# Kernel tuning notes

Measured on AMD Instinct MI355X. Metric: run time of the kernel, lower is better.

The kernel has to match this reference:

```python
import jax, jax.numpy as jnp
import numpy as np

VOCAB, E, HID, T = 100000, 256, 512, 12
H = HID // 2          # per-direction LSTM hidden
B, S = 64, 256
START, STOP = 10, 11  # tag_to_ix['<START>'], tag_to_ix['<STOP>']
NEG = -10000.0


def setup_inputs() -> dict:
    key = jax.random.key(0)
    ks = jax.random.split(key, 16)
    inp = {
        'batch_sentence': jax.random.randint(ks[0], (B, S), 0, VOCAB),
        'sentence_length': S,
        'batch_chars2': jnp.zeros((1,), jnp.int64 if jax.config.jax_enable_x64 else jnp.int32),
        'chars2_length': 1,
        'emb': jax.random.normal(ks[1], (VOCAB, E), jnp.float32),
        # PyTorch LSTM layout: W_ih [4H, in], W_hh [4H, H], gate order i,f,g,o
        'Wih_f': jax.random.normal(ks[2], (4 * H, E), jnp.float32) * 0.05,
        'Whh_f': jax.random.normal(ks[3], (4 * H, H), jnp.float32) * 0.05,
        'bih_f': jnp.zeros((4 * H,), jnp.float32),
        'bhh_f': jnp.zeros((4 * H,), jnp.float32),
        'Wih_b': jax.random.normal(ks[4], (4 * H, E), jnp.float32) * 0.05,
        'Whh_b': jax.random.normal(ks[5], (4 * H, H), jnp.float32) * 0.05,
        'bih_b': jnp.zeros((4 * H,), jnp.float32),
        'bhh_b': jnp.zeros((4 * H,), jnp.float32),
        'Wt': jax.random.normal(ks[6], (T, HID), jnp.float32) * 0.05,
        'bt': jnp.zeros((T,), jnp.float32),
        'transitions': jax.random.normal(ks[7], (T, T), jnp.float32),
        # init_hidden() draws randn hidden state: h0/c0 [2 dirs, B, H]
        'h0': jax.random.normal(ks[8], (2, B, H), jnp.float32),
        'c0': jax.random.normal(ks[9], (2, B, H), jnp.float32),
    }
    return inp


def _lstm(x, h0, c0, Wih, Whh, bih, bhh):
    # x: [S, B, E] -> hs: [S, B, H]
    def step(carry, xt):
        h, c = carry
        g = xt @ Wih.T + h @ Whh.T + (bih + bhh)
        i, f, gg, o = jnp.split(g, 4, axis=-1)
        c = jax.nn.sigmoid(f) * c + jax.nn.sigmoid(i) * jnp.tanh(gg)
        h = jax.nn.sigmoid(o) * jnp.tanh(c)
        return (h, c), h
    _, hs = jax.lax.scan(step, (h0, c0), x)
    return hs


def _viterbi(feats, transitions):
    # feats: [S, T] emissions for one sequence
    init = jnp.full((T,), NEG, feats.dtype).at[START].set(0.0)

    def step(fv, feat):
        scores = fv[None, :] + transitions            # [next_tag, prev_tag]
        new_fv = jnp.max(scores, axis=1) + feat       # best prev per next
        bptr = jnp.argmax(scores, axis=1)
        return new_fv, bptr

    fv, bptrs = jax.lax.scan(step, init, feats)       # bptrs: [S, T]
    term = fv + transitions[STOP]
    term = term.at[STOP].set(NEG).at[START].set(NEG)  # torch code masks these
    last = jnp.argmax(term)
    score = term[last]

    def back(tag, bptr):
        return bptr[tag], tag                          # y_t = tag at time t
    _, path = jax.lax.scan(back, last, bptrs, reverse=True)
    return score, path


def reference(batch_sentence, sentence_length, batch_chars2, chars2_length,
              emb, Wih_f, Whh_f, bih_f, bhh_f, Wih_b, Whh_b, bih_b, bhh_b,
              Wt, bt, transitions, h0, c0):
    # word embeddings (dropout = identity at inference)
    x = emb[batch_sentence].transpose(1, 0, 2)        # [S, B, E]
    hf = _lstm(x, h0[0], c0[0], Wih_f, Whh_f, bih_f, bhh_f)
    hb = _lstm(x[::-1], h0[1], c0[1], Wih_b, Whh_b, bih_b, bhh_b)[::-1]
    out = jnp.concatenate([hf, hb], axis=-1)          # [S, B, HID]
    feats = out @ Wt.T + bt                           # [S, B, T]
    feats = feats.transpose(1, 0, 2)                  # [B, S, T]
    scores, paths = jax.vmap(_viterbi, in_axes=(0, None))(feats, transitions)
    return scores, paths
```

## Files before the change

kernel.cpp:

```cpp
#include <hip/hip_runtime.h>
#include <cstdint>
#include <cstddef>

#define EDIM 256
#define HID  512
#define NTAG 12
#define HDIM 256
#define BB   64
#define SS   256
#define START_TAG 10
#define STOP_TAG  11
#define NEGV (-10000.0f)
#define UPW  8

typedef __attribute__((ext_vector_type(8))) short bf16x8;
typedef __attribute__((ext_vector_type(4))) float f32x4;

__device__ __forceinline__ unsigned short bf16_rne(float x) {
  union { float f; unsigned u; } a; a.f = x;
  return (unsigned short)((a.u + 0x7fffu + ((a.u >> 16) & 1u)) >> 16);
}
__device__ __forceinline__ float bf16_tof(unsigned short h) {
  union { unsigned u; float f; } a; a.u = ((unsigned)h) << 16; return a.f;
}
__device__ __forceinline__ void unpack8(const unsigned* u, bf16x8& hi, bf16x8& lo) {
#pragma unroll
  for (int j = 0; j < 8; ++j) {
    hi[j] = (short)(u[j] & 0xffffu);
    lo[j] = (short)(u[j] >> 16);
  }
}
__device__ __forceinline__ void pack_hilo(const float* xf, bf16x8& hi, bf16x8& lo) {
#pragma unroll
  for (int j = 0; j < 8; ++j) {
    unsigned short hb = bf16_rne(xf[j]);
    hi[j] = (short)hb;
    lo[j] = (short)bf16_rne(xf[j] - bf16_tof(hb));
  }
}

__global__ void k0_gather(const int* __restrict__ sent,
                          const float* __restrict__ emb,
                          unsigned int* __restrict__ xpk) {
  int t = blockIdx.x;
  for (int n = threadIdx.x; n < BB * EDIM; n += 256) {
    int b = n >> 8, k = n & 255;
    int tok = sent[b * SS + t];
    float x = emb[(size_t)tok * EDIM + k];
    unsigned short hb = bf16_rne(x);
    unsigned short lb = bf16_rne(x - bf16_tof(hb));
    xpk[((size_t)t * BB + b) * EDIM + k] = (unsigned)hb | ((unsigned)lb << 16);
  }
}

__global__ void __launch_bounds__(256, 1)
lstm_fused(const float* __restrict__ WhhF, const float* __restrict__ WhhB,
           const float* __restrict__ WihF, const float* __restrict__ WihB,
           const float* __restrict__ bihF, const float* __restrict__ bhhF,
           const float* __restrict__ bihB, const float* __restrict__ bhhB,
           const unsigned int* __restrict__ xpk,
           const float* __restrict__ h0, const float* __restrict__ c0,
           float* __restrict__ hseq, unsigned int* __restrict__ hx) {
  const int bid = blockIdx.x;
  const int d = bid >> 5, w = bid & 31;
  const int tid = threadIdx.x;
  const int lane = tid & 63;
  const int v = tid >> 6;
  const int l15 = lane & 15, l4 = lane >> 4;
  const int bcol = v * 16 + l15;
  const int u2 = ((l4 & 1) << 2) | ((l4 >> 1) << 1);
  const bool low = (l4 < 2);
  const int kg0 = w * UPW + u2;
  const float* Whh = d ? WhhB : WhhF;
  const float* Wih = d ? WihB : WihF;
  const float* bi  = d ? bihB : bihF;
  const float* bh  = d ? bhhB : bhhF;

  bf16x8 Hhi[2][8], Hlo[2][8], Xhi[2][8], Xlo[2][8];
#pragma unroll
  for (int rt = 0; rt < 2; ++rt) {
    int i = rt * 16 + l15;
    int R = ((i >> 3) << 8) + w * UPW + (i & 7);
    const float* wrow = Whh + (size_t)R * HDIM;
    const float* xrow = Wih + (size_t)R * EDIM;
#pragma unroll
    for (int kk = 0; kk < 8; ++kk) {
      {
        float4 f0 = *(const float4*)(wrow + kk * 32 + l4 * 8);
        float4 f1 = *(const float4*)(wrow + kk * 32 + l4 * 8 + 4);
        float xf[8] = {f0.x, f0.y, f0.z, f0.w, f1.x, f1.y, f1.z, f1.w};
        pack_hilo(xf, Hhi[rt][kk], Hlo[rt][kk]);
      }
      {
        float4 f0 = *(const float4*)(xrow + kk * 32 + l4 * 8);
        float4 f1 = *(const float4*)(xrow + kk * 32 + l4 * 8 + 4);
        float xf[8] = {f0.x, f0.y, f0.z, f0.w, f1.x, f1.y, f1.z, f1.w};
        pack_hilo(xf, Xhi[rt][kk], Xlo[rt][kk]);
      }
    }
  }
  f32x4 bias0, bias1;
#pragma unroll
  for (int r = 0; r < 4; ++r) {
    int i0 = l4 * 4 + r;
    int R0 = ((i0 >> 3) << 8) + w * UPW + (i0 & 7);
    bias0[r] = bi[R0] + bh[R0];
    int i1 = 16 + i0;
    int R1 = ((i1 >> 3) << 8) + w * UPW + (i1 & 7);
    bias1[r] = bi[R1] + bh[R1];
  }
  float c2[2];
  c2[0] = c0[((size_t)d * BB + bcol) * HDIM + kg0];
  c2[1] = c0[((size_t)d * BB + bcol) * HDIM + kg0 + 1];

  for (int s = 0; s < SS; ++s) {
    const int t = d ? (SS - 1 - s) : s;

    const unsigned int* xc = xpk + ((size_t)t * BB + bcol) * EDIM;
    uint4 xq[16];
#pragma unroll
    for (int kk = 0; kk < 8; ++kk) {
      xq[2 * kk]     = *(const uint4*)(xc + kk * 32 + l4 * 8);
      xq[2 * kk + 1] = *(const uint4*)(xc + kk * 32 + l4 * 8 + 4);
    }

    f32x4 accA = bias0, accD = bias1;
    f32x4 accB = {0.f, 0.f, 0.f, 0.f}, accC = accB, accE = accB, accF = accB;
#pragma unroll
    for (int kk = 0; kk < 8; ++kk) {
      unsigned u[8] = {xq[2 * kk].x, xq[2 * kk].y, xq[2 * kk].z, xq[2 * kk].w,
                       xq[2 * kk + 1].x, xq[2 * kk + 1].y,
                       xq[2 * kk + 1].z, xq[2 * kk + 1].w};
      bf16x8 xh, xl;
      unpack8(u, xh, xl);
      accA = __builtin_amdgcn_mfma_f32_16x16x32_bf16(Xhi[0][kk], xh, accA, 0, 0, 0);
      accB = __builtin_amdgcn_mfma_f32_16x16x32_bf16(Xhi[0][kk], xl, accB, 0, 0, 0);
      accC = __builtin_amdgcn_mfma_f32_16x16x32_bf16(Xlo[0][kk], xh, accC, 0, 0, 0);
      accD = __builtin_amdgcn_mfma_f32_16x16x32_bf16(Xhi[1][kk], xh, accD, 0, 0, 0);
      accE = __builtin_amdgcn_mfma_f32_16x16x32_bf16(Xhi[1][kk], xl, accE, 0, 0, 0);
      accF = __builtin_amdgcn_mfma_f32_16x16x32_bf16(Xlo[1][kk], xh, accF, 0, 0, 0);
    }

    unsigned uv[64];
    if (s > 0) {
      const unsigned int* slot =
          hx + ((size_t)(d * 4 + ((s - 1) & 3)) * HDIM) * BB + bcol;
      while (true) {
        int bad = 0;
#pragma unroll
        for (int kk = 0; kk < 8; ++kk)
#pragma unroll
          for (int j = 0; j < 8; ++j) {
            unsigned val = __hip_atomic_load(
                slot + (size_t)(kk * 32 + l4 * 8 + j) * BB,
                __ATOMIC_RELAXED, __HIP_MEMORY_SCOPE_AGENT);
            uv[kk * 8 + j] = val;
            bad |= (val == 0xFFFFFFFFu);
          }
        if (!__any(bad)) break;
        __builtin_amdgcn_s_sleep(1);
      }
      __builtin_amdgcn_sched_barrier(0);
    }

    {
      unsigned int* ra =
          hx + ((size_t)(d * 4 + ((s + 1) & 3)) * HDIM) * BB + bcol;
      __hip_atomic_store(ra + (size_t)kg0 * BB, 0xFFFFFFFFu,
                         __ATOMIC_RELAXED, __HIP_MEMORY_SCOPE_AGENT);
      __hip_atomic_store(ra + (size_t)(kg0 + 1) * BB, 0xFFFFFFFFu,
                         __ATOMIC_RELAXED, __HIP_MEMORY_SCOPE_AGENT);
    }

    if (s == 0) {
      const float* hrow = h0 + ((size_t)d * BB + bcol) * HDIM;
#pragma unroll
      for (int kk = 0; kk < 8; ++kk) {
        float4 f0 = *(const float4*)(hrow + kk * 32 + l4 * 8);
        float4 f1 = *(const float4*)(hrow + kk * 32 + l4 * 8 + 4);
        float xf[8] = {f0.x, f0.y, f0.z, f0.w, f1.x, f1.y, f1.z, f1.w};
        bf16x8 bhf, blf;
        pack_hilo(xf, bhf, blf);
        accA = __builtin_amdgcn_mfma_f32_16x16x32_bf16(Hhi[0][kk], bhf, accA, 0, 0, 0);
        accB = __builtin_amdgcn_mfma_f32_16x16x32_bf16(Hhi[0][kk], blf, accB, 0, 0, 0);
        accC = __builtin_amdgcn_mfma_f32_16x16x32_bf16(Hlo[0][kk], bhf, accC, 0, 0, 0);
        accD = __builtin_amdgcn_mfma_f32_16x16x32_bf16(Hhi[1][kk], bhf, accD, 0, 0, 0);
        accE = __builtin_amdgcn_mfma_f32_16x16x32_bf16(Hhi[1][kk], blf, accE, 0, 0, 0);
        accF = __builtin_amdgcn_mfma_f32_16x16x32_bf16(Hlo[1][kk], bhf, accF, 0, 0, 0);
      }
    } else {
#pragma unroll
      for (int kk = 0; kk < 8; ++kk) {
        bf16x8 bhf, blf;
        unpack8(&uv[kk * 8], bhf, blf);
        accA = __builtin_amdgcn_mfma_f32_16x16x32_bf16(Hhi[0][kk], bhf, accA, 0, 0, 0);
        accB = __builtin_amdgcn_mfma_f32_16x16x32_bf16(Hhi[0][kk], blf, accB, 0, 0, 0);
        accC = __builtin_amdgcn_mfma_f32_16x16x32_bf16(Hlo[0][kk], bhf, accC, 0, 0, 0);
        accD = __builtin_amdgcn_mfma_f32_16x16x32_bf16(Hhi[1][kk], bhf, accD, 0, 0, 0);
        accE = __builtin_amdgcn_mfma_f32_16x16x32_bf16(Hhi[1][kk], blf, accE, 0, 0, 0);
        accF = __builtin_amdgcn_mfma_f32_16x16x32_bf16(Hlo[1][kk], bhf, accF, 0, 0, 0);
      }
    }
    f32x4 acc0 = accA + accB + accC;
    f32x4 acc1 = accD + accE + accF;

    f32x4 r0, r1;
#pragma unroll
    for (int r = 0; r < 4; ++r) {
      r0[r] = __shfl_xor(acc0[r], 32);
      r1[r] = __shfl_xor(acc1[r], 32);
    }

    float hn[2]; unsigned pv[2];
#pragma unroll
    for (int e = 0; e < 2; ++e) {
      float iv = low ? acc0[e]     : r0[2 + e];
      float fv = low ? r0[e]       : acc0[2 + e];
      float gv = low ? acc1[e]     : r1[2 + e];
      float ov = low ? r1[e]       : acc1[2 + e];
      float si = 1.f / (1.f + expf(-iv));
      float sf = 1.f / (1.f + expf(-fv));
      float so = 1.f / (1.f + expf(-ov));
      float cn = sf * c2[e] + si * tanhf(gv);
      c2[e] = cn;
      float h = so * tanhf(cn);
      hn[e] = h;
      unsigned short hb2 = bf16_rne(h);
      unsigned short lb2 = bf16_rne(h - bf16_tof(hb2));
      pv[e] = (unsigned)hb2 | ((unsigned)lb2 << 16);
    }

    asm volatile("s_waitcnt vmcnt(0)" ::: "memory");

    {
      unsigned int* pd =
          hx + ((size_t)(d * 4 + (s & 3)) * HDIM) * BB + bcol;
      __hip_atomic_store(pd + (size_t)kg0 * BB, pv[0],
                         __ATOMIC_RELAXED, __HIP_MEMORY_SCOPE_AGENT);
      __hip_atomic_store(pd + (size_t)(kg0 + 1) * BB, pv[1],
                         __ATOMIC_RELAXED, __HIP_MEMORY_SCOPE_AGENT);
    }

    hseq[(((size_t)d * SS + t) * HDIM + kg0) * BB + bcol] = hn[0];
    hseq[(((size_t)d * SS + t) * HDIM + kg0 + 1) * BB + bcol] = hn[1];
  }
}

__global__ void k3_feats(const float* __restrict__ hseq,
                         const float* __restrict__ Wt,
                         const float* __restrict__ bt,
                         float* __restrict__ feats) {
  int t = blockIdx.x, tid = threadIdx.x;
  __shared__ float Wl[NTAG][HID];
  for (int n = tid; n < NTAG * HID; n += 256) Wl[n >> 9][n & 511] = Wt[n];
  __syncthreads();
  int b = tid & 63, tq = tid >> 6;
  float acc[3];
  for (int c = 0; c < 3; ++c) acc[c] = bt[tq * 3 + c];
  const float* hf = hseq + ((size_t)0 * SS + t) * HDIM * BB;
  const float* hb = hseq + ((size_t)1 * SS + t) * HDIM * BB;
  for (int k = 0; k < HDIM; ++k) {
    float h1 = hf[(size_t)k * BB + b];
    float h2 = hb[(size_t)k * BB + b];
#pragma unroll
    for (int c = 0; c < 3; ++c) {
      acc[c] += h1 * Wl[tq * 3 + c][k];
      acc[c] += h2 * Wl[tq * 3 + c][HDIM + k];
    }
  }
  for (int c = 0; c < 3; ++c)
    feats[((size_t)t * BB + b) * NTAG + tq * 3 + c] = acc[c];
}

__global__ void k4_viterbi(const float* __restrict__ feats,
                           const float* __restrict__ trans,
                           float* __restrict__ out) {
  int b = blockIdx.x, lane = threadIdx.x;
  __shared__ float tr[NTAG][NTAG];
  __shared__ float fv[NTAG], fnew[NTAG], term[NTAG];
  __shared__ unsigned char bp[SS][NTAG];
  for (int n = lane; n < NTAG * NTAG; n += 64) tr[n / NTAG][n % NTAG] = trans[n];
  if (lane < NTAG) fv[lane] = (lane == START_TAG) ? 0.f : NEGV;
  __syncthreads();
  for (int s = 0; s < SS; ++s) {
    if (lane < NTAG) {
      float best = fv[0] + tr[lane][0]; int arg = 0;
#pragma unroll
      for (int j = 1; j < NTAG; ++j) {
        float vv = fv[j] + tr[lane][j];
        if (vv > best) { best = vv; arg = j; }
      }
      fnew[lane] = best + feats[((size_t)s * BB + b) * NTAG + lane];
      bp[s][lane] = (unsigned char)arg;
    }
    __syncthreads();
    if (lane < NTAG) fv[lane] = fnew[lane];
    __syncthreads();
  }
  if (lane < NTAG) {
    float vv = fv[lane] + tr[STOP_TAG][lane];
    if (lane == STOP_TAG || lane == START_TAG) vv = NEGV;
    term[lane] = vv;
  }
  __syncthreads();
  if (lane == 0) {
    float best = term[0]; int arg = 0;
    for (int j = 1; j < NTAG; ++j)
      if (term[j] > best) { best = term[j]; arg = j; }
    out[b] = best;
    int cur = arg;
    for (int s = SS - 1; s >= 0; --s) {
      out[64 + (size_t)b * SS + s] = (float)cur;
      cur = bp[s][cur];
    }
  }
}

extern "C" void kernel_launch(void* const* d_in, const int* in_sizes, int n_in,
                              void* d_out, int out_size, void* d_ws, size_t ws_size,
                              hipStream_t stream) {
  (void)in_sizes; (void)n_in; (void)out_size;
  const int*   sent  = (const int*)d_in[0];
  const float* emb   = (const float*)d_in[4];
  const float* WihF  = (const float*)d_in[5];
  const float* WhhF  = (const float*)d_in[6];
  const float* bihF  = (const float*)d_in[7];
  const float* bhhF  = (const float*)d_in[8];
  const float* WihB  = (const float*)d_in[9];
  const float* WhhB  = (const float*)d_in[10];
  const float* bihB  = (const float*)d_in[11];
  const float* bhhB  = (const float*)d_in[12];
  const float* Wt    = (const float*)d_in[13];
  const float* bt    = (const float*)d_in[14];
  const float* trans = (const float*)d_in[15];
  const float* h0    = (const float*)d_in[16];
  const float* c0    = (const float*)d_in[17];
  float* out = (float*)d_out;

  char* ws = (char*)d_ws;
  unsigned int* hx = (unsigned int*)ws;
  unsigned int* xpk = (unsigned int*)(ws + 524288ull);
  float* hseq  = (float*)(ws + 524288ull + 16777216ull);
  float* feats = (float*)(ws + 524288ull + 16777216ull + 33554432ull);
  if (ws_size < 52428800ull) return;

  hipMemsetAsync(hx, 0xFF, 524288ull, stream);
  k0_gather<<<SS, 256, 0, stream>>>(sent, emb, xpk);
  lstm_fused<<<64, 256, 0, stream>>>(WhhF, WhhB, WihF, WihB,
                                     bihF, bhhF, bihB, bhhB,
                                     xpk, h0, c0, hseq, hx);
  k3_feats<<<SS, 256, 0, stream>>>(hseq, Wt, bt, feats);
  k4_viterbi<<<BB, 64, 0, stream>>>(feats, trans, out);
}
```

Baseline: 1.620 ms.

## Prefetch next-step input projection and vectorize hidden-state ring buffer exchange

```diff
diff --git a/kernel.cpp b/kernel.cpp
--- a/kernel.cpp
+++ b/kernel.cpp
@@ -113,24 +113,18 @@
   c2[0] = c0[((size_t)d * BB + bcol) * HDIM + kg0];
   c2[1] = c0[((size_t)d * BB + bcol) * HDIM + kg0 + 1];
 
-  for (int s = 0; s < SS; ++s) {
-    const int t = d ? (SS - 1 - s) : s;
-
-    const unsigned int* xc = xpk + ((size_t)t * BB + bcol) * EDIM;
-    uint4 xq[16];
+  f32x4 accA, accB, accC, accD, accE, accF;
+
+  {
+    const int t0 = d ? (SS - 1) : 0;
+    const unsigned int* xc = xpk + ((size_t)t0 * BB + bcol) * EDIM;
+    accA = bias0; accD = bias1;
+    accB = (f32x4){0.f, 0.f, 0.f, 0.f}; accC = accB; accE = accB; accF = accB;
 #pragma unroll
     for (int kk = 0; kk < 8; ++kk) {
-      xq[2 * kk]     = *(const uint4*)(xc + kk * 32 + l4 * 8);
-      xq[2 * kk + 1] = *(const uint4*)(xc + kk * 32 + l4 * 8 + 4);
-    }
-
-    f32x4 accA = bias0, accD = bias1;
-    f32x4 accB = {0.f, 0.f, 0.f, 0.f}, accC = accB, accE = accB, accF = accB;
-#pragma unroll
-    for (int kk = 0; kk < 8; ++kk) {
-      unsigned u[8] = {xq[2 * kk].x, xq[2 * kk].y, xq[2 * kk].z, xq[2 * kk].w,
-                       xq[2 * kk + 1].x, xq[2 * kk + 1].y,
-                       xq[2 * kk + 1].z, xq[2 * kk + 1].w};
+      uint4 q0 = *(const uint4*)(xc + kk * 32 + l4 * 8);
+      uint4 q1 = *(const uint4*)(xc + kk * 32 + l4 * 8 + 4);
+      unsigned u[8] = {q0.x, q0.y, q0.z, q0.w, q1.x, q1.y, q1.z, q1.w};
       bf16x8 xh, xl;
       unpack8(u, xh, xl);
       accA = __builtin_amdgcn_mfma_f32_16x16x32_bf16(Xhi[0][kk], xh, accA, 0, 0, 0);
@@ -140,23 +134,33 @@
       accE = __builtin_amdgcn_mfma_f32_16x16x32_bf16(Xhi[1][kk], xl, accE, 0, 0, 0);
       accF = __builtin_amdgcn_mfma_f32_16x16x32_bf16(Xlo[1][kk], xh, accF, 0, 0, 0);
     }
-
-    unsigned uv[64];
+  }
+
+  unsigned int* ringd = hx + (size_t)d * 4 * 16384;
+
+  for (int s = 0; s < SS; ++s) {
+    const int t = d ? (SS - 1 - s) : s;
+
+    uint4 uq[16];
     if (s > 0) {
-      const unsigned int* slot =
-          hx + ((size_t)(d * 4 + ((s - 1) & 3)) * HDIM) * BB + bcol;
+      const unsigned int* slotp = ringd + (size_t)((s - 1) & 3) * 16384;
       while (true) {
+#pragma unroll
+        for (int kk = 0; kk < 8; ++kk) {
+          const unsigned int* p = slotp + ((kk * 4 + l4) * 64 + bcol) * 8;
+          asm volatile("global_load_dwordx4 %0, %1, off sc1"
+                       : "=v"(uq[2 * kk]) : "v"(p));
+          asm volatile("global_load_dwordx4 %0, %1, off sc1"
+                       : "=v"(uq[2 * kk + 1]) : "v"(p + 4));
+        }
+        asm volatile("s_waitcnt vmcnt(0)" ::: "memory");
+        __builtin_amdgcn_sched_barrier(0);
         int bad = 0;
 #pragma unroll
-        for (int kk = 0; kk < 8; ++kk)
-#pragma unroll
-          for (int j = 0; j < 8; ++j) {
-            unsigned val = __hip_atomic_load(
-                slot + (size_t)(kk * 32 + l4 * 8 + j) * BB,
-                __ATOMIC_RELAXED, __HIP_MEMORY_SCOPE_AGENT);
-            uv[kk * 8 + j] = val;
-            bad |= (val == 0xFFFFFFFFu);
-          }
+        for (int q = 0; q < 16; ++q) {
+          bad |= (uq[q].x == 0xFFFFFFFFu) | (uq[q].y == 0xFFFFFFFFu) |
+                 (uq[q].z == 0xFFFFFFFFu) | (uq[q].w == 0xFFFFFFFFu);
+        }
         if (!__any(bad)) break;
         __builtin_amdgcn_s_sleep(1);
       }
@@ -164,11 +168,10 @@
     }
 
     {
-      unsigned int* ra =
-          hx + ((size_t)(d * 4 + ((s + 1) & 3)) * HDIM) * BB + bcol;
-      __hip_atomic_store(ra + (size_t)kg0 * BB, 0xFFFFFFFFu,
-                         __ATOMIC_RELAXED, __HIP_MEMORY_SCOPE_AGENT);
-      __hip_atomic_store(ra + (size_t)(kg0 + 1) * BB, 0xFFFFFFFFu,
+      unsigned long long* ra = (unsigned long long*)(
+          ringd + (size_t)((s + 1) & 3) * 16384) +
+          ((size_t)w * 64 + bcol) * 4 + (u2 >> 1);
+      __hip_atomic_store(ra, 0xFFFFFFFFFFFFFFFFull,
                          __ATOMIC_RELAXED, __HIP_MEMORY_SCOPE_AGENT);
     }
 
@@ -191,8 +194,11 @@
     } else {
 #pragma unroll
       for (int kk = 0; kk < 8; ++kk) {
+        unsigned u[8] = {uq[2 * kk].x, uq[2 * kk].y, uq[2 * kk].z, uq[2 * kk].w,
+                         uq[2 * kk + 1].x, uq[2 * kk + 1].y,
+                         uq[2 * kk + 1].z, uq[2 * kk + 1].w};
         bf16x8 bhf, blf;
-        unpack8(&uv[kk * 8], bhf, blf);
+        unpack8(u, bhf, blf);
         accA = __builtin_amdgcn_mfma_f32_16x16x32_bf16(Hhi[0][kk], bhf, accA, 0, 0, 0);
         accB = __builtin_amdgcn_mfma_f32_16x16x32_bf16(Hhi[0][kk], blf, accB, 0, 0, 0);
         accC = __builtin_amdgcn_mfma_f32_16x16x32_bf16(Hlo[0][kk], bhf, accC, 0, 0, 0);
@@ -233,16 +239,37 @@
     asm volatile("s_waitcnt vmcnt(0)" ::: "memory");
 
     {
-      unsigned int* pd =
-          hx + ((size_t)(d * 4 + (s & 3)) * HDIM) * BB + bcol;
-      __hip_atomic_store(pd + (size_t)kg0 * BB, pv[0],
-                         __ATOMIC_RELAXED, __HIP_MEMORY_SCOPE_AGENT);
-      __hip_atomic_store(pd + (size_t)(kg0 + 1) * BB, pv[1],
-                         __ATOMIC_RELAXED, __HIP_MEMORY_SCOPE_AGENT);
+      unsigned long long pv64 =
+          (unsigned long long)pv[0] | ((unsigned long long)pv[1] << 32);
+      unsigned long long* pd = (unsigned long long*)(
+          ringd + (size_t)(s & 3) * 16384) +
+          ((size_t)w * 64 + bcol) * 4 + (u2 >> 1);
+      __hip_atomic_store(pd, pv64, __ATOMIC_RELAXED, __HIP_MEMORY_SCOPE_AGENT);
     }
 
     hseq[(((size_t)d * SS + t) * HDIM + kg0) * BB + bcol] = hn[0];
     hseq[(((size_t)d * SS + t) * HDIM + kg0 + 1) * BB + bcol] = hn[1];
+
+    if (s + 1 < SS) {
+      const int tn = d ? (SS - 2 - s) : (s + 1);
+      const unsigned int* xc = xpk + ((size_t)tn * BB + bcol) * EDIM;
+      accA = bias0; accD = bias1;
+      accB = (f32x4){0.f, 0.f, 0.f, 0.f}; accC = accB; accE = accB; accF = accB;
+#pragma unroll
+      for (int kk = 0; kk < 8; ++kk) {
+        uint4 q0 = *(const uint4*)(xc + kk * 32 + l4 * 8);
+        uint4 q1 = *(const uint4*)(xc + kk * 32 + l4 * 8 + 4);
+        unsigned u[8] = {q0.x, q0.y, q0.z, q0.w, q1.x, q1.y, q1.z, q1.w};
+        bf16x8 xh, xl;
+        unpack8(u, xh, xl);
+        accA = __builtin_amdgcn_mfma_f32_16x16x32_bf16(Xhi[0][kk], xh, accA, 0, 0, 0);
+        accB = __builtin_amdgcn_mfma_f32_16x16x32_bf16(Xhi[0][kk], xl, accB, 0, 0, 0);
+        accC = __builtin_amdgcn_mfma_f32_16x16x32_bf16(Xlo[0][kk], xh, accC, 0, 0, 0);
+        accD = __builtin_amdgcn_mfma_f32_16x16x32_bf16(Xhi[1][kk], xh, accD, 0, 0, 0);
+        accE = __builtin_amdgcn_mfma_f32_16x16x32_bf16(Xhi[1][kk], xl, accE, 0, 0, 0);
+        accF = __builtin_amdgcn_mfma_f32_16x16x32_bf16(Xlo[1][kk], xh, accF, 0, 0, 0);
+      }
+    }
   }
 }
 
```

Measured after the change: 1.593 ms. About the same (-1.6%).
